# Kernel tuning notes

Measured on AMD Instinct MI355X. Metric: run time of the kernel, lower is better.

## Reference

```python
import jax, jax.numpy as jnp
import numpy as np

B, R, S = 4, 65536, 48  # batch, rays (256x256), depth_resolution


def setup_inputs() -> dict:
    key = jax.random.key(0)
    k1, k2, k3 = jax.random.split(key, 3)
    colors = jax.random.uniform(k1, (B, R, S, 3), dtype=jnp.float32)
    densities = jax.random.normal(k2, (B, R, S, 1), dtype=jnp.float32)
    # stratified depths in [-1, 1], monotone along sample axis (axis=-2)
    depths = jnp.sort(
        jax.random.uniform(k3, (B, R, S, 1), dtype=jnp.float32) * 2.0 - 1.0,
        axis=-2,
    )
    return {"colors": colors, "densities": densities, "depths": depths}


def reference(colors, densities, depths):
    # MipRayMarcher2.run_forward
    deltas = depths[:, :, 1:] - depths[:, :, :-1]                     # [B,R,S-1,1]
    colors_mid = (colors[:, :, :-1] + colors[:, :, 1:]) * 0.5         # [B,R,S-1,3]
    densities_mid = (densities[:, :, :-1] + densities[:, :, 1:]) * 0.5
    depths_mid = (depths[:, :, :-1] + depths[:, :, 1:]) * 0.5

    densities_mid = jax.nn.softplus(densities_mid - 1.0)
    density_delta = densities_mid * deltas
    alpha = 1.0 - jnp.exp(-density_delta)                             # [B,R,S-1,1]

    # exclusive cumulative transmittance along the sample axis
    alpha_shifted = jnp.concatenate(
        [jnp.ones_like(alpha[:, :, :1]), 1.0 - alpha + 1e-10], axis=-2
    )
    weights = alpha * jnp.cumprod(alpha_shifted, axis=-2)[:, :, :-1]  # [B,R,S-1,1]

    composite_rgb = jnp.sum(weights * colors_mid, axis=-2)            # [B,R,3]
    weight_total = jnp.sum(weights, axis=2)                           # [B,R,1]
    composite_depth = jnp.sum(weights * depths_mid, axis=-2) / weight_total
    composite_depth = jnp.nan_to_num(composite_depth, nan=jnp.inf)
    composite_depth = jnp.clip(composite_depth, jnp.min(depths), jnp.max(depths))

    composite_rgb = composite_rgb * 2.0 - 1.0
    return composite_rgb, composite_depth, weights
```

## Files before the change

kernel.cpp:

```cpp
#include <hip/hip_runtime.h>
#include <math.h>


#define S_SAMPLES 48
#define S_INTERVALS 47
#define WR 16
#define RSTRIDE 52
#define WAVES 2
#define BT (WAVES * 64)
#define WAVE_LDS (2 * WR * RSTRIDE)

__global__ __launch_bounds__(BT, 5) void raymarch_kernel(
    const float* __restrict__ colors,
    const float* __restrict__ densities,
    const float* __restrict__ depths,
    float* __restrict__ out_rgb,
    float* __restrict__ out_depth,
    float* __restrict__ out_w,
    int nRays) {
    __shared__ float4 smem4[WAVES * WAVE_LDS / 4];
    const int wid = threadIdx.x >> 6;
    const int lane = threadIdx.x & 63;
    float* A = (float*)smem4 + wid * WAVE_LDS;
    float* B = A + WR * RSTRIDE;

    const int waveId = blockIdx.x * WAVES + wid;
    const size_t wray = (size_t)waveId * WR;

    {
        const float4* gdep = (const float4*)(depths + wray * S_SAMPLES);
        const float4* gden = (const float4*)(densities + wray * S_SAMPLES);
#pragma unroll
        for (int k = 0; k < 3; ++k) {
            int fidx = lane + k * 64;
            int rr = fidx / 12;
            int i4 = fidx - rr * 12;
            *(float4*)&A[rr * RSTRIDE + i4 * 4] = gdep[fidx];
            *(float4*)&B[rr * RSTRIDE + i4 * 4] = gden[fidx];
        }
        if (lane < WR) {
            float4 z = make_float4(0.f, 0.f, 0.f, 0.f);
            *(float4*)&A[lane * RSTRIDE + 48] = z;
            *(float4*)&B[lane * RSTRIDE + 48] = z;
        }
    }

    const int r = lane >> 2;
    const int q = lane & 3;
    const int rbase = r * RSTRIDE;
    const int base = rbase + 12 * q;

    const float4* gcol4 = (const float4*)(colors + wray * (S_SAMPLES * 3));
    const int f0 = lane, f1 = lane + 64, f2 = lane + 128;
    const int rr0 = f0 / 12, i40 = f0 - rr0 * 12;
    const int rr1 = f1 / 12, i41 = f1 - rr1 * 12;
    const int rr2 = f2 / 12, i42 = f2 - rr2 * 12;
    float4 t0 = gcol4[rr0 * 36 + i40];
    float4 t1 = gcol4[rr1 * 36 + i41];
    float4 t2 = gcol4[rr2 * 36 + i42];

    asm volatile("" ::: "memory");

    const float4 dA = *(const float4*)&A[base + 0];
    const float4 dB4 = *(const float4*)&A[base + 4];
    const float4 dC = *(const float4*)&A[base + 8];
    const float dD = A[base + 12];
    const float4 nA = *(const float4*)&B[base + 0];
    const float4 nB4 = *(const float4*)&B[base + 4];
    const float4 nC = *(const float4*)&B[base + 8];
    const float nD = B[base + 12];

    const float LOG2E = 1.4426950408889634f;

    float g0, g1, g2, g3, g4, g5, g6, g7, g8, g9, g10, g11;
#define DD(dP, dN, nP, nN, OUT, HAS)                                   \
    do {                                                               \
        float xs = (0.5f * ((nP) + (nN)) - 1.f) * LOG2E;               \
        float sp2 = fmaxf(xs, 0.f) + log2f(1.f + exp2f(-fabsf(xs)));   \
        OUT = (HAS) ? ((dN) - (dP)) * sp2 : 0.f;                       \
    } while (0)
    DD(dA.x, dA.y, nA.x, nA.y, g0, true);
    DD(dA.y, dA.z, nA.y, nA.z, g1, true);
    DD(dA.z, dA.w, nA.z, nA.w, g2, true);
    DD(dA.w, dB4.x, nA.w, nB4.x, g3, true);
    DD(dB4.x, dB4.y, nB4.x, nB4.y, g4, true);
    DD(dB4.y, dB4.z, nB4.y, nB4.z, g5, true);
    DD(dB4.z, dB4.w, nB4.z, nB4.w, g6, true);
    DD(dB4.w, dC.x, nB4.w, nC.x, g7, true);
    DD(dC.x, dC.y, nC.x, nC.y, g8, true);
    DD(dC.y, dC.z, nC.y, nC.z, g9, true);
    DD(dC.z, dC.w, nC.z, nC.w, g10, true);
    DD(dC.w, dD, nC.w, nD, g11, (q < 3));
#undef DD

    float S1 = g0, S2 = S1 + g1, S3 = S2 + g2, S4 = S3 + g3;
    float S5 = S4 + g4, S6 = S5 + g5, S7 = S6 + g6, S8 = S7 + g7;
    float S9 = S8 + g8, S10 = S9 + g9, S11 = S10 + g10, S12 = S11 + g11;

    float Sloc = S12;
    float u1s = __shfl_up(Sloc, 1);
    float ps = (q >= 1) ? Sloc + u1s : Sloc;
    float u2s = __shfl_up(ps, 2);
    float incl = (q >= 2) ? ps + u2s : ps;
    float u3s = __shfl_up(incl, 1);
    float Sexc = (q >= 1) ? u3s : 0.f;

    float Tp = exp2f(-Sexc);
    float T1 = exp2f(-(Sexc + S1)), T2 = exp2f(-(Sexc + S2));
    float T3 = exp2f(-(Sexc + S3)), T4 = exp2f(-(Sexc + S4));
    float T5 = exp2f(-(Sexc + S5)), T6 = exp2f(-(Sexc + S6));
    float T7 = exp2f(-(Sexc + S7)), T8 = exp2f(-(Sexc + S8));
    float T9 = exp2f(-(Sexc + S9)), T10 = exp2f(-(Sexc + S10));
    float T11 = exp2f(-(Sexc + S11)), T12 = exp2f(-(Sexc + S12));
    float W0 = Tp - T1, W1 = T1 - T2, W2 = T2 - T3, W3 = T3 - T4;
    float W4 = T4 - T5, W5 = T5 - T6, W6 = T6 - T7, W7 = T7 - T8;
    float W8 = T8 - T9, W9 = T9 - T10, W10 = T10 - T11, W11 = T11 - T12;

    float ad = 0.f;
    ad = fmaf(W0, 0.5f * (dA.x + dA.y), ad);
    ad = fmaf(W1, 0.5f * (dA.y + dA.z), ad);
    ad = fmaf(W2, 0.5f * (dA.z + dA.w), ad);
    ad = fmaf(W3, 0.5f * (dA.w + dB4.x), ad);
    ad = fmaf(W4, 0.5f * (dB4.x + dB4.y), ad);
    ad = fmaf(W5, 0.5f * (dB4.y + dB4.z), ad);
    ad = fmaf(W6, 0.5f * (dB4.z + dB4.w), ad);
    ad = fmaf(W7, 0.5f * (dB4.w + dC.x), ad);
    ad = fmaf(W8, 0.5f * (dC.x + dC.y), ad);
    ad = fmaf(W9, 0.5f * (dC.y + dC.z), ad);
    ad = fmaf(W10, 0.5f * (dC.z + dC.w), ad);
    ad = fmaf(W11, 0.5f * (dC.w + dD), ad);
    float aw = Tp - T12;

    asm volatile("" ::: "memory");
    *(float4*)&A[base + 0] = make_float4(W0, W1, W2, W3);
    *(float4*)&A[base + 4] = make_float4(W4, W5, W6, W7);
    *(float4*)&A[base + 8] = make_float4(W8, W9, W10, W11);

#pragma unroll
    for (int off = 1; off <= 2; off <<= 1) {
        aw += __shfl_xor(aw, off);
        ad += __shfl_xor(ad, off);
    }
    float lastDep = __shfl(dC.w, lane | 3);
    float firstDep = __shfl(dA.x, lane & ~3);
    if (q == 0) {
        float d = ad / aw;
        d = fminf(fmaxf(d, firstDep), lastDep);
        out_depth[wray + r] = d;
    }

    asm volatile("" : "+v"(t0.x), "+v"(t0.y), "+v"(t0.z), "+v"(t0.w),
                      "+v"(t1.x), "+v"(t1.y), "+v"(t1.z), "+v"(t1.w),
                      "+v"(t2.x), "+v"(t2.y), "+v"(t2.z), "+v"(t2.w));

    float Wm1 = __shfl_up(W11, 1);
    if (q == 0) Wm1 = 0.f;
    float v0 = 0.5f * (Wm1 + W0), v1 = 0.5f * (W0 + W1);
    float v2 = 0.5f * (W1 + W2), v3 = 0.5f * (W2 + W3);
    float v4 = 0.5f * (W3 + W4), v5 = 0.5f * (W4 + W5);
    float v6 = 0.5f * (W5 + W6), v7 = 0.5f * (W6 + W7);
    float v8 = 0.5f * (W7 + W8), v9 = 0.5f * (W8 + W9);
    float v10 = 0.5f * (W9 + W10), v11 = 0.5f * (W10 + W11);

    asm volatile("" ::: "memory");

    {
        float* gw = out_w + wray * S_INTERVALS;
#pragma unroll
        for (int k = 0; k < 12; ++k) {
            int g = lane + k * 64;
            if (g < WR * S_INTERVALS) {
                int ray = g / S_INTERVALS;
                int s = g - ray * S_INTERVALS;
                gw[g] = A[ray * RSTRIDE + s];
            }
        }
    }

    float a0 = 0.f, a1 = 0.f, a2 = 0.f;

#define ACC4(vA, vB, vC, vD, fa, fb, fc)                                \
    do {                                                                \
        a0 = fmaf(vA, (fa).x, a0); a1 = fmaf(vA, (fa).y, a1);           \
        a2 = fmaf(vA, (fa).z, a2); a0 = fmaf(vB, (fa).w, a0);           \
        a1 = fmaf(vB, (fb).x, a1); a2 = fmaf(vB, (fb).y, a2);           \
        a0 = fmaf(vC, (fb).z, a0); a1 = fmaf(vC, (fb).w, a1);           \
        a2 = fmaf(vC, (fc).x, a2); a0 = fmaf(vD, (fc).y, a0);           \
        a1 = fmaf(vD, (fc).z, a1); a2 = fmaf(vD, (fc).w, a2);           \
    } while (0)
#define LD3(f, loc)                                                     \
    float4 f##a = *(const float4*)&B[rbase + (loc)];                    \
    float4 f##b = *(const float4*)&B[rbase + (loc) + 4];                \
    float4 f##c = *(const float4*)&B[rbase + (loc) + 8];

#pragma unroll
    for (int c = 0; c < 3; ++c) {
        asm volatile("" ::: "memory");
        *(float4*)&B[rr0 * RSTRIDE + i40 * 4] = t0;
        *(float4*)&B[rr1 * RSTRIDE + i41 * 4] = t1;
        *(float4*)&B[rr2 * RSTRIDE + i42 * 4] = t2;
        if (c < 2) {
            t0 = gcol4[rr0 * 36 + (c + 1) * 12 + i40];
            t1 = gcol4[rr1 * 36 + (c + 1) * 12 + i41];
            t2 = gcol4[rr2 * 36 + (c + 1) * 12 + i42];
        }
        asm volatile("" ::: "memory");
        if (c == 0) {
            if (q == 0) {
                LD3(x, 0) LD3(y, 12) LD3(z, 24)
                ACC4(v0, v1, v2, v3, xa, xb, xc);
                ACC4(v4, v5, v6, v7, ya, yb, yc);
                ACC4(v8, v9, v10, v11, za, zb, zc);
            } else if (q == 1) {
                LD3(x, 36)
                ACC4(v0, v1, v2, v3, xa, xb, xc);
            }
        } else if (c == 1) {
            if (q == 1) {
                LD3(x, 0) LD3(y, 12)
                ACC4(v4, v5, v6, v7, xa, xb, xc);
                ACC4(v8, v9, v10, v11, ya, yb, yc);
            } else if (q == 2) {
                LD3(x, 24) LD3(y, 36)
                ACC4(v0, v1, v2, v3, xa, xb, xc);
                ACC4(v4, v5, v6, v7, ya, yb, yc);
            }
        } else {
            if (q == 2) {
                LD3(x, 0)
                ACC4(v8, v9, v10, v11, xa, xb, xc);
            } else if (q == 3) {
                LD3(x, 12) LD3(y, 24) LD3(z, 36)
                ACC4(v0, v1, v2, v3, xa, xb, xc);
                ACC4(v4, v5, v6, v7, ya, yb, yc);
                ACC4(v8, v9, v10, v11, za, zb, zc);
            }
        }
    }
#undef LD3
#undef ACC4

#pragma unroll
    for (int off = 1; off <= 2; off <<= 1) {
        a0 += __shfl_xor(a0, off);
        a1 += __shfl_xor(a1, off);
        a2 += __shfl_xor(a2, off);
    }
    if (q == 0) {
        size_t rb = (wray + r) * 3;
        out_rgb[rb + 0] = fmaf(a0, 2.f, -1.f);
        out_rgb[rb + 1] = fmaf(a1, 2.f, -1.f);
        out_rgb[rb + 2] = fmaf(a2, 2.f, -1.f);
    }
}

extern "C" void kernel_launch(void* const* d_in, const int* in_sizes, int n_in,
                              void* d_out, int out_size, void* d_ws, size_t ws_size,
                              hipStream_t stream) {
    const float* colors = (const float*)d_in[0];
    const float* densities = (const float*)d_in[1];
    const float* depths = (const float*)d_in[2];

    const int nRays = in_sizes[2] / S_SAMPLES;
    const int nWaves = nRays / WR;
    const int nBlocks = nWaves / WAVES;

    float* out = (float*)d_out;
    float* out_rgb = out;
    float* out_depth = out + (size_t)nRays * 3;
    float* out_w = out + (size_t)nRays * 4;

    raymarch_kernel<<<nBlocks, BT, 0, stream>>>(
        colors, densities, depths, out_rgb, out_depth, out_w, nRays);
}
```

Measured before the change: 54.14 us.

## Issue all color loads upfront before compute and relax occupancy bound

All nine per-lane float4 color loads are now issued at kernel start, before the depth/density staging and weight computation, instead of being prefetched one third at a time inside the accumulation loop. This puts every global read in flight at once to hide memory latency behind the transmittance math. The extra 24 live registers per lane are paid for by lowering the launch-bounds occupancy hint from 5 to 4 blocks per CU, which risks lower occupancy.

Result: faster. 51.99 us (median of 2 runs) (-4.0%).

```diff
diff --git a/kernel.cpp b/kernel.cpp
--- a/kernel.cpp
+++ b/kernel.cpp
@@ -10,7 +10,7 @@
 #define BT (WAVES * 64)
 #define WAVE_LDS (2 * WR * RSTRIDE)
 
-__global__ __launch_bounds__(BT, 5) void raymarch_kernel(
+__global__ __launch_bounds__(BT, 4) void raymarch_kernel(
     const float* __restrict__ colors,
     const float* __restrict__ densities,
     const float* __restrict__ depths,
@@ -27,9 +27,24 @@
     const int waveId = blockIdx.x * WAVES + wid;
     const size_t wray = (size_t)waveId * WR;
 
+    const float4* gdep = (const float4*)(depths + wray * S_SAMPLES);
+    const float4* gden = (const float4*)(densities + wray * S_SAMPLES);
+    const float4* gcol4 = (const float4*)(colors + wray * (S_SAMPLES * 3));
+    const int rr0 = lane / 12, i40 = lane - rr0 * 12;
+    const int f1 = lane + 64, rr1 = f1 / 12, i41 = f1 - rr1 * 12;
+    const int f2 = lane + 128, rr2 = f2 / 12, i42 = f2 - rr2 * 12;
+
+    float4 u0 = gcol4[rr0 * 36 + i40];
+    float4 u1 = gcol4[rr1 * 36 + i41];
+    float4 u2 = gcol4[rr2 * 36 + i42];
+    float4 u3 = gcol4[rr0 * 36 + 12 + i40];
+    float4 u4 = gcol4[rr1 * 36 + 12 + i41];
+    float4 u5 = gcol4[rr2 * 36 + 12 + i42];
+    float4 u6 = gcol4[rr0 * 36 + 24 + i40];
+    float4 u7 = gcol4[rr1 * 36 + 24 + i41];
+    float4 u8 = gcol4[rr2 * 36 + 24 + i42];
+
     {
-        const float4* gdep = (const float4*)(depths + wray * S_SAMPLES);
-        const float4* gden = (const float4*)(densities + wray * S_SAMPLES);
 #pragma unroll
         for (int k = 0; k < 3; ++k) {
             int fidx = lane + k * 64;
@@ -49,15 +64,6 @@
     const int q = lane & 3;
     const int rbase = r * RSTRIDE;
     const int base = rbase + 12 * q;
-
-    const float4* gcol4 = (const float4*)(colors + wray * (S_SAMPLES * 3));
-    const int f0 = lane, f1 = lane + 64, f2 = lane + 128;
-    const int rr0 = f0 / 12, i40 = f0 - rr0 * 12;
-    const int rr1 = f1 / 12, i41 = f1 - rr1 * 12;
-    const int rr2 = f2 / 12, i42 = f2 - rr2 * 12;
-    float4 t0 = gcol4[rr0 * 36 + i40];
-    float4 t1 = gcol4[rr1 * 36 + i41];
-    float4 t2 = gcol4[rr2 * 36 + i42];
 
     asm volatile("" ::: "memory");
 
@@ -149,9 +155,15 @@
         out_depth[wray + r] = d;
     }
 
-    asm volatile("" : "+v"(t0.x), "+v"(t0.y), "+v"(t0.z), "+v"(t0.w),
-                      "+v"(t1.x), "+v"(t1.y), "+v"(t1.z), "+v"(t1.w),
-                      "+v"(t2.x), "+v"(t2.y), "+v"(t2.z), "+v"(t2.w));
+    asm volatile("" : "+v"(u0.x), "+v"(u0.y), "+v"(u0.z), "+v"(u0.w),
+                      "+v"(u1.x), "+v"(u1.y), "+v"(u1.z), "+v"(u1.w),
+                      "+v"(u2.x), "+v"(u2.y), "+v"(u2.z), "+v"(u2.w),
+                      "+v"(u3.x), "+v"(u3.y), "+v"(u3.z), "+v"(u3.w));
+    asm volatile("" : "+v"(u4.x), "+v"(u4.y), "+v"(u4.z), "+v"(u4.w),
+                      "+v"(u5.x), "+v"(u5.y), "+v"(u5.z), "+v"(u5.w),
+                      "+v"(u6.x), "+v"(u6.y), "+v"(u6.z), "+v"(u6.w),
+                      "+v"(u7.x), "+v"(u7.y), "+v"(u7.z), "+v"(u7.w),
+                      "+v"(u8.x), "+v"(u8.y), "+v"(u8.z), "+v"(u8.w));
 
     float Wm1 = __shfl_up(W11, 1);
     if (q == 0) Wm1 = 0.f;
@@ -192,51 +204,50 @@
     float4 f##a = *(const float4*)&B[rbase + (loc)];                    \
     float4 f##b = *(const float4*)&B[rbase + (loc) + 4];                \
     float4 f##c = *(const float4*)&B[rbase + (loc) + 8];
-
-#pragma unroll
-    for (int c = 0; c < 3; ++c) {
-        asm volatile("" ::: "memory");
-        *(float4*)&B[rr0 * RSTRIDE + i40 * 4] = t0;
-        *(float4*)&B[rr1 * RSTRIDE + i41 * 4] = t1;
-        *(float4*)&B[rr2 * RSTRIDE + i42 * 4] = t2;
-        if (c < 2) {
-            t0 = gcol4[rr0 * 36 + (c + 1) * 12 + i40];
-            t1 = gcol4[rr1 * 36 + (c + 1) * 12 + i41];
-            t2 = gcol4[rr2 * 36 + (c + 1) * 12 + i42];
-        }
-        asm volatile("" ::: "memory");
-        if (c == 0) {
-            if (q == 0) {
-                LD3(x, 0) LD3(y, 12) LD3(z, 24)
-                ACC4(v0, v1, v2, v3, xa, xb, xc);
-                ACC4(v4, v5, v6, v7, ya, yb, yc);
-                ACC4(v8, v9, v10, v11, za, zb, zc);
-            } else if (q == 1) {
-                LD3(x, 36)
-                ACC4(v0, v1, v2, v3, xa, xb, xc);
-            }
-        } else if (c == 1) {
-            if (q == 1) {
-                LD3(x, 0) LD3(y, 12)
-                ACC4(v4, v5, v6, v7, xa, xb, xc);
-                ACC4(v8, v9, v10, v11, ya, yb, yc);
-            } else if (q == 2) {
-                LD3(x, 24) LD3(y, 36)
-                ACC4(v0, v1, v2, v3, xa, xb, xc);
-                ACC4(v4, v5, v6, v7, ya, yb, yc);
-            }
-        } else {
-            if (q == 2) {
-                LD3(x, 0)
-                ACC4(v8, v9, v10, v11, xa, xb, xc);
-            } else if (q == 3) {
-                LD3(x, 12) LD3(y, 24) LD3(z, 36)
-                ACC4(v0, v1, v2, v3, xa, xb, xc);
-                ACC4(v4, v5, v6, v7, ya, yb, yc);
-                ACC4(v8, v9, v10, v11, za, zb, zc);
-            }
-        }
-    }
+#define STAGE(pa, pb, pc)                                               \
+    do {                                                                \
+        *(float4*)&B[rr0 * RSTRIDE + i40 * 4] = pa;                     \
+        *(float4*)&B[rr1 * RSTRIDE + i41 * 4] = pb;                     \
+        *(float4*)&B[rr2 * RSTRIDE + i42 * 4] = pc;                     \
+    } while (0)
+
+    asm volatile("" ::: "memory");
+    STAGE(u0, u1, u2);
+    asm volatile("" ::: "memory");
+    if (q == 0) {
+        LD3(x, 0) LD3(y, 12) LD3(z, 24)
+        ACC4(v0, v1, v2, v3, xa, xb, xc);
+        ACC4(v4, v5, v6, v7, ya, yb, yc);
+        ACC4(v8, v9, v10, v11, za, zb, zc);
+    } else if (q == 1) {
+        LD3(x, 36)
+        ACC4(v0, v1, v2, v3, xa, xb, xc);
+    }
+    asm volatile("" ::: "memory");
+    STAGE(u3, u4, u5);
+    asm volatile("" ::: "memory");
+    if (q == 1) {
+        LD3(x, 0) LD3(y, 12)
+        ACC4(v4, v5, v6, v7, xa, xb, xc);
+        ACC4(v8, v9, v10, v11, ya, yb, yc);
+    } else if (q == 2) {
+        LD3(x, 24) LD3(y, 36)
+        ACC4(v0, v1, v2, v3, xa, xb, xc);
+        ACC4(v4, v5, v6, v7, ya, yb, yc);
+    }
+    asm volatile("" ::: "memory");
+    STAGE(u6, u7, u8);
+    asm volatile("" ::: "memory");
+    if (q == 2) {
+        LD3(x, 0)
+        ACC4(v8, v9, v10, v11, xa, xb, xc);
+    } else if (q == 3) {
+        LD3(x, 12) LD3(y, 24) LD3(z, 36)
+        ACC4(v0, v1, v2, v3, xa, xb, xc);
+        ACC4(v4, v5, v6, v7, ya, yb, yc);
+        ACC4(v8, v9, v10, v11, za, zb, zc);
+    }
+#undef STAGE
 #undef LD3
 #undef ACC4
 
```
